# Performance work log

Hardware: AMD Instinct MI355X
Metric: run time of the kernel (lower is better)

Reference implementation:

```python
import jax, jax.numpy as jnp
import numpy as np
import math

B, C, DH = 2048, 64, 512
CAP_VOCAB = 11  # max(core_capacities)+1
DIST_VOCAB = 3


def setup_inputs() -> dict:
    key = jax.random.key(0)
    ks = jax.random.split(key, 12)
    inp = {
        "Ht_C": jax.random.normal(ks[0], (B, C, DH), jnp.float32),
        "core_capacities": jax.random.randint(ks[1], (B, C), 0, CAP_VOCAB),
        "distances": jax.random.randint(ks[2], (B, C), 0, DIST_VOCAB),
        "H_X": jax.random.normal(ks[3], (B, DH), jnp.float32),
        "Ht_S": jax.random.normal(ks[4], (B, DH), jnp.float32),
        "Eq_Q": jax.random.normal(ks[5], (B, DH), jnp.float32),
        "double": jax.random.randint(ks[6], (B,), 0, 2).astype(bool),
        # learned parameters (nn.Embedding tables and bias-free Linear weights, [out,in])
        "cap_emb": jax.random.normal(ks[7], (CAP_VOCAB, DH), jnp.float32) * 0.02,
        "dist_emb": jax.random.normal(ks[8], (DIST_VOCAB, DH), jnp.float32) * 0.02,
        "W_q": jax.random.normal(ks[9], (DH, 3 * DH), jnp.float32) * (1.0 / math.sqrt(3 * DH)),
        "W_k": jax.random.normal(ks[10], (DH, DH), jnp.float32) * (1.0 / math.sqrt(DH)),
        "W_v": jax.random.normal(ks[11], (DH, DH), jnp.float32) * (1.0 / math.sqrt(DH)),
    }
    return inp


def reference(Ht_C, core_capacities, distances, H_X, Ht_S, Eq_Q, double,
              cap_emb, dist_emb, W_q, W_k, W_v):
    scale = 1.0 / math.sqrt(Ht_C.shape[-1])  # 1/sqrt(d_H), slice_emb_size == d_H
    # dynamic core embeddings G_{t,q}^{(C)}: [B,C,dH]
    G = Ht_C + cap_emb[core_capacities] + dist_emb[distances]
    # context and projections
    context = jnp.concatenate([H_X, Ht_S, Eq_Q], axis=-1)          # [B,3dH]
    Q = context @ W_q.T                                            # [B,dH]
    K = jnp.einsum('bcd,ed->bce', G, W_k)                          # [B,C,dH]
    V = jnp.einsum('bcd,ed->bce', G, W_v)                          # [B,C,dH]
    # glimpse attention over cores
    attn_logits = jnp.einsum('bcd,bd->bc', K, Q) * scale           # [B,C]
    attn_weights = jax.nn.softmax(attn_logits, axis=-1)            # softmax over cores
    glimpse = jnp.einsum('bc,bcd->bd', attn_weights, V)            # [B,dH]
    # pointer logits + capacity mask
    u = jnp.einsum('bcd,bd->bc', K, glimpse) * scale               # [B,C]
    need = jnp.where(double[:, None], 2, 1)                        # [B,1]
    invalid = core_capacities < need                               # [B,C]
    u = jnp.where(invalid, -jnp.inf, u)
    return jax.nn.softmax(u, axis=-1)                              # [B,C]
```

## Files before the change

### kernel.cpp

```cpp
#include <hip/hip_runtime.h>
#include <math.h>

#define DH 512
#define CC 64
#define NB 2048
#define SCALE 0.044194173824159216f

#define PD(d) ((((d) >> 5) * 36) + ((d) & 31))

__device__ __forceinline__ float wsum(float v) {
#pragma unroll
  for (int off = 32; off; off >>= 1) v += __shfl_xor(v, off, 64);
  return v;
}

__global__ __launch_bounds__(128) void pre_kernel(const float* __restrict__ Wq,
                                                  const float* __restrict__ Wv,
                                                  const float* __restrict__ Wk,
                                                  float* __restrict__ Aout,
                                                  float* __restrict__ Mout,
                                                  const unsigned char* __restrict__ dbl,
                                                  int* __restrict__ need) {
  const int bx = blockIdx.x;
  const int t = threadIdx.x;
  if (bx == 256) {
    __shared__ int flagNZ, flagFP;
    if (t == 0) { flagNZ = 0; flagFP = 0; }
    __syncthreads();
    int nz = 0, fp = 0;
    for (int i = t; i < NB; i += 128) {
      if (i & 3) {
        unsigned char v = dbl[i];
        nz |= (v != 0);
        fp |= (v == 0x3f) | (v == 0x80);
      }
    }
    if (nz) atomicOr(&flagNZ, 1);
    if (fp) atomicOr(&flagFP, 1);
    __syncthreads();
    const int isFP = flagFP, isByte = flagNZ && !flagFP;
    for (int i = t; i < NB; i += 128) {
      int v;
      if (isFP)        v = (((const float*)dbl)[i] != 0.0f);
      else if (isByte) v = (dbl[i] != 0);
      else             v = (((const int*)dbl)[i] != 0);
      need[i] = v ? 2 : 1;
    }
    return;
  }
  __shared__ float As[16][64];
  __shared__ float Bs[16][64];
  const int mt = bx >> 3, nt = bx & 7;
  const int m0 = mt * 64, n0 = nt * 64;
  const bool isQ = (m0 < 1536);
  const float* Acol = isQ ? (Wq + m0) : (Wv + (m0 - 1536));
  const int lda = isQ ? 1536 : 512;
  float* Cout = isQ ? (Aout + (size_t)m0 * 512) : (Mout + (size_t)(m0 - 1536) * 512);
  const int lr = t >> 3;
  const int lc = (t & 7) << 3;
  const int tx = t & 15, ty = t >> 4;

  float4 ra0, ra1, rb0, rb1;
  ra0 = *(const float4*)&Acol[(size_t)lr * lda + lc];
  ra1 = *(const float4*)&Acol[(size_t)lr * lda + lc + 4];
  rb0 = *(const float4*)&Wk[(size_t)lr * 512 + n0 + lc];
  rb1 = *(const float4*)&Wk[(size_t)lr * 512 + n0 + lc + 4];
  float acc[8][4] = {};
  for (int k0 = 0; k0 < 512; k0 += 16) {
    __syncthreads();
    *(float4*)&As[lr][lc] = ra0;
    *(float4*)&As[lr][lc + 4] = ra1;
    *(float4*)&Bs[lr][lc] = rb0;
    *(float4*)&Bs[lr][lc + 4] = rb1;
    __syncthreads();
    if (k0 + 16 < 512) {
      const int kn = k0 + 16 + lr;
      ra0 = *(const float4*)&Acol[(size_t)kn * lda + lc];
      ra1 = *(const float4*)&Acol[(size_t)kn * lda + lc + 4];
      rb0 = *(const float4*)&Wk[(size_t)kn * 512 + n0 + lc];
      rb1 = *(const float4*)&Wk[(size_t)kn * 512 + n0 + lc + 4];
    }
#pragma unroll
    for (int k = 0; k < 16; ++k) {
      float4 a0 = *(float4*)&As[k][ty << 3];
      float4 a1 = *(float4*)&As[k][(ty << 3) + 4];
      float4 b  = *(float4*)&Bs[k][tx << 2];
      float av[8] = {a0.x, a0.y, a0.z, a0.w, a1.x, a1.y, a1.z, a1.w};
      float bv[4] = {b.x, b.y, b.z, b.w};
#pragma unroll
      for (int i = 0; i < 8; ++i)
#pragma unroll
        for (int j = 0; j < 4; ++j) acc[i][j] = fmaf(av[i], bv[j], acc[i][j]);
    }
  }
#pragma unroll
  for (int i = 0; i < 8; ++i) {
    float4 o = {acc[i][0], acc[i][1], acc[i][2], acc[i][3]};
    *(float4*)&Cout[(size_t)((ty << 3) + i) * 512 + n0 + (tx << 2)] = o;
  }
}

#define AS_STR 132

__global__ __launch_bounds__(256) void gemm_nn2p(const float* __restrict__ A0,
                                                 const float* __restrict__ A1,
                                                 const float* __restrict__ A2,
                                                 const float* __restrict__ B,
                                                 float* __restrict__ Cp,
                                                 int kchunk) {
  __shared__ float As[16 * AS_STR];
  __shared__ float Bs[16 * 64];
  const int t = threadIdx.x;
  const int m0 = blockIdx.x * 128, n0 = blockIdx.y * 64;
  const int kbeg = blockIdx.z * kchunk, kend = kbeg + kchunk;
  float* C = Cp + (size_t)blockIdx.z * (NB * DH);
  const int tx = t & 15, ty = t >> 4;
  const int ar0 = t >> 2;
  const int ak4 = (t & 3) << 2;
  const int bk = t >> 4, bn4 = (t & 15) << 2;

  float4 ra0, ra1, rb;
  {
    const float* base = (kbeg < 512) ? A0 : ((kbeg < 1024) ? A1 : A2);
    const int kk = kbeg & 511;
    ra0 = *(const float4*)&base[(size_t)(m0 + ar0) * 512 + kk + ak4];
    ra1 = *(const float4*)&base[(size_t)(m0 + ar0 + 64) * 512 + kk + ak4];
    rb  = *(const float4*)&B[(size_t)(kbeg + bk) * 512 + n0 + bn4];
  }
  float acc[8][4] = {};
  for (int k0 = kbeg; k0 < kend; k0 += 16) {
    __syncthreads();
    As[(ak4 + 0) * AS_STR + ar0] = ra0.x;
    As[(ak4 + 1) * AS_STR + ar0] = ra0.y;
    As[(ak4 + 2) * AS_STR + ar0] = ra0.z;
    As[(ak4 + 3) * AS_STR + ar0] = ra0.w;
    As[(ak4 + 0) * AS_STR + ar0 + 64] = ra1.x;
    As[(ak4 + 1) * AS_STR + ar0 + 64] = ra1.y;
    As[(ak4 + 2) * AS_STR + ar0 + 64] = ra1.z;
    As[(ak4 + 3) * AS_STR + ar0 + 64] = ra1.w;
    *(float4*)&Bs[bk * 64 + bn4] = rb;
    __syncthreads();
    if (k0 + 16 < kend) {
      const int kn = k0 + 16;
      const float* base = (kn < 512) ? A0 : ((kn < 1024) ? A1 : A2);
      const int kk = kn & 511;
      ra0 = *(const float4*)&base[(size_t)(m0 + ar0) * 512 + kk + ak4];
      ra1 = *(const float4*)&base[(size_t)(m0 + ar0 + 64) * 512 + kk + ak4];
      rb  = *(const float4*)&B[(size_t)(kn + bk) * 512 + n0 + bn4];
    }
#pragma unroll
    for (int k = 0; k < 16; ++k) {
      float4 a0 = *(float4*)&As[k * AS_STR + (ty << 3)];
      float4 a1 = *(float4*)&As[k * AS_STR + (ty << 3) + 4];
      float4 b  = *(float4*)&Bs[k * 64 + (tx << 2)];
      float av[8] = {a0.x, a0.y, a0.z, a0.w, a1.x, a1.y, a1.z, a1.w};
      float bv[4] = {b.x, b.y, b.z, b.w};
#pragma unroll
      for (int i = 0; i < 8; ++i)
#pragma unroll
        for (int j = 0; j < 4; ++j) acc[i][j] = fmaf(av[i], bv[j], acc[i][j]);
    }
  }
#pragma unroll
  for (int i = 0; i < 8; ++i) {
    float4 o = {acc[i][0], acc[i][1], acc[i][2], acc[i][3]};
    *(float4*)&C[(size_t)(m0 + (ty << 3) + i) * 512 + n0 + (tx << 2)] = o;
  }
}

__global__ __launch_bounds__(256)
__attribute__((amdgpu_waves_per_eu(2)))
void fused_kernel(const float* __restrict__ HtC,
                  const int* __restrict__ caps,
                  const int* __restrict__ dists,
                  const float* __restrict__ Qkp,
                  const float* __restrict__ Mm,
                  const float* __restrict__ cap_emb,
                  const float* __restrict__ dist_emb,
                  const int* __restrict__ need,
                  float* __restrict__ out) {
  const int t = threadIdx.x;
  const int wv = t >> 6, ln = t & 63;
  const int g = ln >> 4, l16 = ln & 15;
  const int b0 = blockIdx.x << 2;

  __shared__ __align__(16) float qk[4][576];
  __shared__ __align__(16) float gks[4][576];
  __shared__ __align__(16) float accs[4][576];
  __shared__ __align__(16) float Gws[4][DH];
  __shared__ __align__(16) float gkp[2][4][DH];
  __shared__ float ec[CC];
  __shared__ float capQ[4][11], distQ[4][3];
  __shared__ float capE[11], distE[3];
  __shared__ float capG[4][11], distG[4][3];
  __shared__ float lsum_s;
  __shared__ int capsS[4][CC], distsS[4][CC];

  {
    const int hh = t >> 6, c = t & 63;
    capsS[hh][c] = caps[(size_t)(b0 + hh) * CC + c];
    distsS[hh][c] = dists[(size_t)(b0 + hh) * CC + c];
  }

  {
    const int hh = t >> 6;
    const int d0 = (t & 63) << 3;
    const size_t bo = (size_t)(b0 + hh) * DH + d0;
    float4 q0 = make_float4(0.f, 0.f, 0.f, 0.f);
    float4 q1 = make_float4(0.f, 0.f, 0.f, 0.f);
#pragma unroll
    for (int z = 0; z < 4; ++z) {
      float4 a = *(const float4*)&Qkp[(size_t)z * NB * DH + bo];
      float4 b4 = *(const float4*)&Qkp[(size_t)z * NB * DH + bo + 4];
      q0.x += a.x; q0.y += a.y; q0.z += a.z; q0.w += a.w;
      q1.x += b4.x; q1.y += b4.y; q1.z += b4.z; q1.w += b4.w;
    }
    *(float4*)&qk[hh][PD(d0)] = q0;
    *(float4*)&qk[hh][PD(d0 + 4)] = q1;
  }
  __syncthreads();

#pragma unroll
  for (int h = 0; h < 4; ++h) {
#pragma unroll
    for (int r = 0; r < 3; ++r) {
      int v = wv + (r << 2);
      if (v < 11) {
        float s = 0.f;
#pragma unroll
        for (int j = 0; j < 8; ++j)
          s = fmaf(cap_emb[v * DH + ln + (j << 6)], qk[h][PD(ln + (j << 6))], s);
        s = wsum(s);
        if (ln == 0) capQ[h][v] = s;
      }
    }
    if (wv < 3) {
      float s = 0.f;
#pragma unroll
      for (int j = 0; j < 8; ++j)
        s = fmaf(dist_emb[wv * DH + ln + (j << 6)], qk[h][PD(ln + (j << 6))], s);
      s = wsum(s);
      if (ln == 0) distQ[h][wv] = s;
    }
  }

  const int coff = l16 << 5;

  for (int h = 0; h < 4; ++h) {
    const int b = b0 + h;
    if (t < 11) capE[t] = 0.f;
    if (t < 3) distE[t] = 0.f;
    __syncthreads();
    float4 qs[8];
#pragma unroll
    for (int j = 0; j < 8; ++j) qs[j] = *(const float4*)&qk[h][l16 * 36 + 4 * j];
    float4 ac[8];
#pragma unroll
    for (int j = 0; j < 8; ++j) ac[j] = make_float4(0.f, 0.f, 0.f, 0.f);
    const float* hb = HtC + (size_t)b * CC * DH;
    float4 hv[8];
    {
      const float* hp = hb + (size_t)((wv << 4) + g) * DH + coff;
#pragma unroll
      for (int j = 0; j < 8; ++j) hv[j] = *(const float4*)&hp[4 * j];
    }
#pragma unroll 1
    for (int k = 0; k < 4; ++k) {
      const int c = (wv << 4) + (k << 2) + g;
      float4 hvn[8];
      if (k < 3) {
        const float* hp = hb + (size_t)(c + 4) * DH + coff;
#pragma unroll
        for (int j = 0; j < 8; ++j) hvn[j] = *(const float4*)&hp[4 * j];
      }
      float s = 0.f;
#pragma unroll
      for (int j = 0; j < 8; ++j) {
        s = fmaf(hv[j].x, qs[j].x, s); s = fmaf(hv[j].y, qs[j].y, s);
        s = fmaf(hv[j].z, qs[j].z, s); s = fmaf(hv[j].w, qs[j].w, s);
      }
      s += __shfl_xor(s, 1, 64);
      s += __shfl_xor(s, 2, 64);
      s += __shfl_xor(s, 4, 64);
      s += __shfl_xor(s, 8, 64);
      float e = __expf(SCALE * (s + capQ[h][capsS[h][c]] + distQ[h][distsS[h][c]]));
      if (l16 == 0) ec[c] = e;
#pragma unroll
      for (int j = 0; j < 8; ++j) {
        ac[j].x = fmaf(e, hv[j].x, ac[j].x); ac[j].y = fmaf(e, hv[j].y, ac[j].y);
        ac[j].z = fmaf(e, hv[j].z, ac[j].z); ac[j].w = fmaf(e, hv[j].w, ac[j].w);
      }
      if (k < 3) {
#pragma unroll
        for (int j = 0; j < 8; ++j) hv[j] = hvn[j];
      }
    }
#pragma unroll
    for (int j = 0; j < 8; ++j) {
      ac[j].x += __shfl_xor(ac[j].x, 16, 64); ac[j].x += __shfl_xor(ac[j].x, 32, 64);
      ac[j].y += __shfl_xor(ac[j].y, 16, 64); ac[j].y += __shfl_xor(ac[j].y, 32, 64);
      ac[j].z += __shfl_xor(ac[j].z, 16, 64); ac[j].z += __shfl_xor(ac[j].z, 32, 64);
      ac[j].w += __shfl_xor(ac[j].w, 16, 64); ac[j].w += __shfl_xor(ac[j].w, 32, 64);
    }
    if (g == 0) {
#pragma unroll
      for (int j = 0; j < 8; ++j)
        *(float4*)&accs[wv][l16 * 36 + 4 * j] = ac[j];
    }
    __syncthreads();
    if (t < CC) {
      float e = ec[t];
      float l = wsum(e);
      if (t == 0) lsum_s = l;
      atomicAdd(&capE[capsS[h][t]], e);
      atomicAdd(&distE[distsS[h][t]], e);
    }
    __syncthreads();
    const float rinv = 1.0f / lsum_s;
#pragma unroll
    for (int dd = 0; dd < 2; ++dd) {
      int d = t + (dd << 8);
      float gg = accs[0][PD(d)] + accs[1][PD(d)] + accs[2][PD(d)] + accs[3][PD(d)];
#pragma unroll
      for (int v = 0; v < 11; ++v) gg = fmaf(capE[v], cap_emb[v * DH + d], gg);
#pragma unroll
      for (int v = 0; v < 3; ++v) gg = fmaf(distE[v], dist_emb[v * DH + d], gg);
      Gws[h][d] = gg * rinv;
    }
    __syncthreads();
  }

  {
    const int e4 = (t & 127) << 2;
    const int half = t >> 7;
    const float* Mp = Mm + (size_t)(half << 8) * DH + e4;
    const float* gw0 = &Gws[0][half << 8];
    const float* gw1 = &Gws[1][half << 8];
    const float* gw2 = &Gws[2][half << 8];
    const float* gw3 = &Gws[3][half << 8];
    float4 s0 = make_float4(0.f, 0.f, 0.f, 0.f);
    float4 s1 = s0, s2 = s0, s3 = s0;
#pragma unroll 4
    for (int d = 0; d < 256; ++d) {
      float4 m4 = *(const float4*)&Mp[(size_t)d * DH];
      float g0 = gw0[d], g1 = gw1[d], g2 = gw2[d], g3 = gw3[d];
      s0.x = fmaf(g0, m4.x, s0.x); s0.y = fmaf(g0, m4.y, s0.y);
      s0.z = fmaf(g0, m4.z, s0.z); s0.w = fmaf(g0, m4.w, s0.w);
      s1.x = fmaf(g1, m4.x, s1.x); s1.y = fmaf(g1, m4.y, s1.y);
      s1.z = fmaf(g1, m4.z, s1.z); s1.w = fmaf(g1, m4.w, s1.w);
      s2.x = fmaf(g2, m4.x, s2.x); s2.y = fmaf(g2, m4.y, s2.y);
      s2.z = fmaf(g2, m4.z, s2.z); s2.w = fmaf(g2, m4.w, s2.w);
      s3.x = fmaf(g3, m4.x, s3.x); s3.y = fmaf(g3, m4.y, s3.y);
      s3.z = fmaf(g3, m4.z, s3.z); s3.w = fmaf(g3, m4.w, s3.w);
    }
    *(float4*)&gkp[half][0][e4] = s0;
    *(float4*)&gkp[half][1][e4] = s1;
    *(float4*)&gkp[half][2][e4] = s2;
    *(float4*)&gkp[half][3][e4] = s3;
  }
  __syncthreads();
#pragma unroll
  for (int h = 0; h < 4; ++h) {
    gks[h][PD(t)] = gkp[0][h][t] + gkp[1][h][t];
    gks[h][PD(t + 256)] = gkp[0][h][t + 256] + gkp[1][h][t + 256];
  }
  __syncthreads();

#pragma unroll
  for (int h = 0; h < 4; ++h) {
#pragma unroll
    for (int r = 0; r < 3; ++r) {
      int v = wv + (r << 2);
      if (v < 11) {
        float s = 0.f;
#pragma unroll
        for (int j = 0; j < 8; ++j)
          s = fmaf(cap_emb[v * DH + ln + (j << 6)], gks[h][PD(ln + (j << 6))], s);
        s = wsum(s);
        if (ln == 0) capG[h][v] = s;
      }
    }
    if (wv < 3) {
      float s = 0.f;
#pragma unroll
      for (int j = 0; j < 8; ++j)
        s = fmaf(dist_emb[wv * DH + ln + (j << 6)], gks[h][PD(ln + (j << 6))], s);
      s = wsum(s);
      if (ln == 0) distG[h][wv] = s;
    }
  }
  __syncthreads();

  for (int h = 3; h >= 0; --h) {
    const int b = b0 + h;
    float4 gs[8];
#pragma unroll
    for (int j = 0; j < 8; ++j) gs[j] = *(const float4*)&gks[h][l16 * 36 + 4 * j];
    const float* hb = HtC + (size_t)b * CC * DH;
    float4 hv[8];
    {
      const float* hp = hb + (size_t)((wv << 4) + g) * DH + coff;
#pragma unroll
      for (int j = 0; j < 8; ++j) hv[j] = *(const float4*)&hp[4 * j];
    }
#pragma unroll 1
    for (int k = 0; k < 4; ++k) {
      const int c = (wv << 4) + (k << 2) + g;
      float4 hvn[8];
      if (k < 3) {
        const float* hp = hb + (size_t)(c + 4) * DH + coff;
#pragma unroll
        for (int j = 0; j < 8; ++j) hvn[j] = *(const float4*)&hp[4 * j];
      }
      float s = 0.f;
#pragma unroll
      for (int j = 0; j < 8; ++j) {
        s = fmaf(hv[j].x, gs[j].x, s); s = fmaf(hv[j].y, gs[j].y, s);
        s = fmaf(hv[j].z, gs[j].z, s); s = fmaf(hv[j].w, gs[j].w, s);
      }
      s += __shfl_xor(s, 1, 64);
      s += __shfl_xor(s, 2, 64);
      s += __shfl_xor(s, 4, 64);
      s += __shfl_xor(s, 8, 64);
      if (l16 == 0)
        ec[c] = SCALE * (s + capG[h][capsS[h][c]] + distG[h][distsS[h][c]]);
      if (k < 3) {
#pragma unroll
        for (int j = 0; j < 8; ++j) hv[j] = hvn[j];
      }
    }
    __syncthreads();
    if (t < CC) {
      int nb = need[b];
      float x = ec[t];
      if (capsS[h][t] < nb) x = -INFINITY;
      float m = x;
#pragma unroll
      for (int off = 32; off; off >>= 1) m = fmaxf(m, __shfl_xor(m, off, 64));
      float e = __expf(x - m);
      float ssum = wsum(e);
      out[(size_t)b * CC + t] = e / ssum;
    }
    __syncthreads();
  }
}

extern "C" void kernel_launch(void* const* d_in, const int* in_sizes, int n_in,
                              void* d_out, int out_size, void* d_ws, size_t ws_size,
                              hipStream_t stream) {
  const float* HtC      = (const float*)d_in[0];
  const int* caps       = (const int*)d_in[1];
  const int* dists      = (const int*)d_in[2];
  const float* H_X      = (const float*)d_in[3];
  const float* Ht_S     = (const float*)d_in[4];
  const float* Eq_Q     = (const float*)d_in[5];
  const unsigned char* dbl = (const unsigned char*)d_in[6];
  const float* cap_emb  = (const float*)d_in[7];
  const float* dist_emb = (const float*)d_in[8];
  const float* W_q      = (const float*)d_in[9];
  const float* W_k      = (const float*)d_in[10];
  const float* W_v      = (const float*)d_in[11];
  float* out = (float*)d_out;

  float* ws     = (float*)d_ws;
  float* wsA    = ws;
  float* wsM    = wsA + 1536 * 512;
  float* wsQkp  = wsM + 512 * 512;
  int* wsNeed   = (int*)(wsQkp + 4 * 2048 * 512);

  pre_kernel<<<257, 128, 0, stream>>>(W_q, W_v, W_k, wsA, wsM, dbl, wsNeed);
  gemm_nn2p<<<dim3(16, 8, 4), 256, 0, stream>>>(H_X, Ht_S, Eq_Q, wsA, wsQkp, 384);
  fused_kernel<<<NB / 4, 256, 0, stream>>>(HtC, caps, dists, wsQkp, wsM,
                                           cap_emb, dist_emb, wsNeed, out);
}
```

Before: 534.1 us.

## Process two batches per block with higher occupancy and split dot-product accumulators

Each fused_kernel block now handles two batch rows instead of four, doubling the grid and cutting shared memory per block, and the waves-per-EU hint rises from 2 to 4 so more blocks can be resident and hide latency on the HtC streaming loads. The per-core dot products use four independent accumulators to shorten the FMA dependency chain. The capacity and distance bias lookups are hoisted out of the inner loop. The cost is that each block reuses its M matrix row loads across only two batches instead of four in the G·M projection, raising global/L2 traffic for M, and register pressure under the tighter occupancy target may cause spills.

Measured after the change: 699.8 us. +31.0%, slower.

```diff
diff --git a/kernel.cpp b/kernel.cpp
--- a/kernel.cpp
+++ b/kernel.cpp
@@ -169,7 +169,7 @@
 }
 
 __global__ __launch_bounds__(256)
-__attribute__((amdgpu_waves_per_eu(2)))
+__attribute__((amdgpu_waves_per_eu(4)))
 void fused_kernel(const float* __restrict__ HtC,
                   const int* __restrict__ caps,
                   const int* __restrict__ dists,
@@ -182,46 +182,42 @@
   const int t = threadIdx.x;
   const int wv = t >> 6, ln = t & 63;
   const int g = ln >> 4, l16 = ln & 15;
-  const int b0 = blockIdx.x << 2;
-
-  __shared__ __align__(16) float qk[4][576];
-  __shared__ __align__(16) float gks[4][576];
+  const int b0 = blockIdx.x << 1;
+
+  __shared__ __align__(16) float qk[2][576];
+  __shared__ __align__(16) float gks[2][576];
   __shared__ __align__(16) float accs[4][576];
-  __shared__ __align__(16) float Gws[4][DH];
-  __shared__ __align__(16) float gkp[2][4][DH];
+  __shared__ __align__(16) float Gws[2][DH];
+  __shared__ __align__(16) float gkp[2][2][DH];
   __shared__ float ec[CC];
-  __shared__ float capQ[4][11], distQ[4][3];
+  __shared__ float capQ[2][11], distQ[2][3];
   __shared__ float capE[11], distE[3];
-  __shared__ float capG[4][11], distG[4][3];
+  __shared__ float capG[2][11], distG[2][3];
   __shared__ float lsum_s;
-  __shared__ int capsS[4][CC], distsS[4][CC];
-
-  {
+  __shared__ int capsS[2][CC], distsS[2][CC];
+
+  if (t < 128) {
     const int hh = t >> 6, c = t & 63;
     capsS[hh][c] = caps[(size_t)(b0 + hh) * CC + c];
     distsS[hh][c] = dists[(size_t)(b0 + hh) * CC + c];
   }
 
   {
-    const int hh = t >> 6;
-    const int d0 = (t & 63) << 3;
+    const int hh = t >> 7;
+    const int d0 = (t & 127) << 2;
     const size_t bo = (size_t)(b0 + hh) * DH + d0;
     float4 q0 = make_float4(0.f, 0.f, 0.f, 0.f);
-    float4 q1 = make_float4(0.f, 0.f, 0.f, 0.f);
 #pragma unroll
     for (int z = 0; z < 4; ++z) {
       float4 a = *(const float4*)&Qkp[(size_t)z * NB * DH + bo];
-      float4 b4 = *(const float4*)&Qkp[(size_t)z * NB * DH + bo + 4];
       q0.x += a.x; q0.y += a.y; q0.z += a.z; q0.w += a.w;
-      q1.x += b4.x; q1.y += b4.y; q1.z += b4.z; q1.w += b4.w;
     }
     *(float4*)&qk[hh][PD(d0)] = q0;
-    *(float4*)&qk[hh][PD(d0 + 4)] = q1;
   }
   __syncthreads();
 
 #pragma unroll
-  for (int h = 0; h < 4; ++h) {
+  for (int h = 0; h < 2; ++h) {
 #pragma unroll
     for (int r = 0; r < 3; ++r) {
       int v = wv + (r << 2);
@@ -246,11 +242,17 @@
 
   const int coff = l16 << 5;
 
-  for (int h = 0; h < 4; ++h) {
+  for (int h = 0; h < 2; ++h) {
     const int b = b0 + h;
     if (t < 11) capE[t] = 0.f;
     if (t < 3) distE[t] = 0.f;
     __syncthreads();
+    float cd[4];
+#pragma unroll
+    for (int k = 0; k < 4; ++k) {
+      const int c = (wv << 4) + (k << 2) + g;
+      cd[k] = capQ[h][capsS[h][c]] + distQ[h][distsS[h][c]];
+    }
     float4 qs[8];
 #pragma unroll
     for (int j = 0; j < 8; ++j) qs[j] = *(const float4*)&qk[h][l16 * 36 + 4 * j];
@@ -273,17 +275,24 @@
 #pragma unroll
         for (int j = 0; j < 8; ++j) hvn[j] = *(const float4*)&hp[4 * j];
       }
-      float s = 0.f;
-#pragma unroll
-      for (int j = 0; j < 8; ++j) {
-        s = fmaf(hv[j].x, qs[j].x, s); s = fmaf(hv[j].y, qs[j].y, s);
-        s = fmaf(hv[j].z, qs[j].z, s); s = fmaf(hv[j].w, qs[j].w, s);
-      }
+      float s0 = 0.f, s1 = 0.f, s2 = 0.f, s3 = 0.f;
+#pragma unroll
+      for (int j = 0; j < 2; ++j) {
+        s0 = fmaf(hv[j].x, qs[j].x, s0); s0 = fmaf(hv[j].y, qs[j].y, s0);
+        s0 = fmaf(hv[j].z, qs[j].z, s0); s0 = fmaf(hv[j].w, qs[j].w, s0);
+        s1 = fmaf(hv[j + 2].x, qs[j + 2].x, s1); s1 = fmaf(hv[j + 2].y, qs[j + 2].y, s1);
+        s1 = fmaf(hv[j + 2].z, qs[j + 2].z, s1); s1 = fmaf(hv[j + 2].w, qs[j + 2].w, s1);
+        s2 = fmaf(hv[j + 4].x, qs[j + 4].x, s2); s2 = fmaf(hv[j + 4].y, qs[j + 4].y, s2);
+        s2 = fmaf(hv[j + 4].z, qs[j + 4].z, s2); s2 = fmaf(hv[j + 4].w, qs[j + 4].w, s2);
+        s3 = fmaf(hv[j + 6].x, qs[j + 6].x, s3); s3 = fmaf(hv[j + 6].y, qs[j + 6].y, s3);
+        s3 = fmaf(hv[j + 6].z, qs[j + 6].z, s3); s3 = fmaf(hv[j + 6].w, qs[j + 6].w, s3);
+      }
+      float s = (s0 + s1) + (s2 + s3);
       s += __shfl_xor(s, 1, 64);
       s += __shfl_xor(s, 2, 64);
       s += __shfl_xor(s, 4, 64);
       s += __shfl_xor(s, 8, 64);
-      float e = __expf(SCALE * (s + capQ[h][capsS[h][c]] + distQ[h][distsS[h][c]]));
+      float e = __expf(SCALE * (s + cd[k]));
       if (l16 == 0) ec[c] = e;
 #pragma unroll
       for (int j = 0; j < 8; ++j) {
@@ -334,40 +343,33 @@
     const int e4 = (t & 127) << 2;
     const int half = t >> 7;
     const float* Mp = Mm + (size_t)(half << 8) * DH + e4;
-    const float* gw0 = &Gws[0][half << 8];
-    const float* gw1 = &Gws[1][half << 8];
-    const float* gw2 = &Gws[2][half << 8];
-    const float* gw3 = &Gws[3][half << 8];
+    const float* g0p = &Gws[0][half << 8];
+    const float* g1p = &Gws[1][half << 8];
     float4 s0 = make_float4(0.f, 0.f, 0.f, 0.f);
-    float4 s1 = s0, s2 = s0, s3 = s0;
-#pragma unroll 4
+    float4 s1 = s0;
+#pragma unroll 8
     for (int d = 0; d < 256; ++d) {
       float4 m4 = *(const float4*)&Mp[(size_t)d * DH];
-      float g0 = gw0[d], g1 = gw1[d], g2 = gw2[d], g3 = gw3[d];
+      float g0 = g0p[d];
+      float g1 = g1p[d];
       s0.x = fmaf(g0, m4.x, s0.x); s0.y = fmaf(g0, m4.y, s0.y);
       s0.z = fmaf(g0, m4.z, s0.z); s0.w = fmaf(g0, m4.w, s0.w);
       s1.x = fmaf(g1, m4.x, s1.x); s1.y = fmaf(g1, m4.y, s1.y);
       s1.z = fmaf(g1, m4.z, s1.z); s1.w = fmaf(g1, m4.w, s1.w);
-      s2.x = fmaf(g2, m4.x, s2.x); s2.y = fmaf(g2, m4.y, s2.y);
-      s2.z = fmaf(g2, m4.z, s2.z); s2.w = fmaf(g2, m4.w, s2.w);
-      s3.x = fmaf(g3, m4.x, s3.x); s3.y = fmaf(g3, m4.y, s3.y);
-      s3.z = fmaf(g3, m4.z, s3.z); s3.w = fmaf(g3, m4.w, s3.w);
     }
     *(float4*)&gkp[half][0][e4] = s0;
     *(float4*)&gkp[half][1][e4] = s1;
-    *(float4*)&gkp[half][2][e4] = s2;
-    *(float4*)&gkp[half][3][e4] = s3;
   }
   __syncthreads();
 #pragma unroll
-  for (int h = 0; h < 4; ++h) {
+  for (int h = 0; h < 2; ++h) {
     gks[h][PD(t)] = gkp[0][h][t] + gkp[1][h][t];
     gks[h][PD(t + 256)] = gkp[0][h][t + 256] + gkp[1][h][t + 256];
   }
   __syncthreads();
 
 #pragma unroll
-  for (int h = 0; h < 4; ++h) {
+  for (int h = 0; h < 2; ++h) {
 #pragma unroll
     for (int r = 0; r < 3; ++r) {
       int v = wv + (r << 2);
@@ -391,8 +393,14 @@
   }
   __syncthreads();
 
-  for (int h = 3; h >= 0; --h) {
+  for (int h = 1; h >= 0; --h) {
     const int b = b0 + h;
+    float cd[4];
+#pragma unroll
+    for (int k = 0; k < 4; ++k) {
+      const int c = (wv << 4) + (k << 2) + g;
+      cd[k] = capG[h][capsS[h][c]] + distG[h][distsS[h][c]];
+    }
     float4 gs[8];
 #pragma unroll
     for (int j = 0; j < 8; ++j) gs[j] = *(const float4*)&gks[h][l16 * 36 + 4 * j];
@@ -412,18 +420,25 @@
 #pragma unroll
         for (int j = 0; j < 8; ++j) hvn[j] = *(const float4*)&hp[4 * j];
       }
-      float s = 0.f;
-#pragma unroll
-      for (int j = 0; j < 8; ++j) {
-        s = fmaf(hv[j].x, gs[j].x, s); s = fmaf(hv[j].y, gs[j].y, s);
-        s = fmaf(hv[j].z, gs[j].z, s); s = fmaf(hv[j].w, gs[j].w, s);
-      }
+      float s0 = 0.f, s1 = 0.f, s2 = 0.f, s3 = 0.f;
+#pragma unroll
+      for (int j = 0; j < 2; ++j) {
+        s0 = fmaf(hv[j].x, gs[j].x, s0); s0 = fmaf(hv[j].y, gs[j].y, s0);
+        s0 = fmaf(hv[j].z, gs[j].z, s0); s0 = fmaf(hv[j].w, gs[j].w, s0);
+        s1 = fmaf(hv[j + 2].x, gs[j + 2].x, s1); s1 = fmaf(hv[j + 2].y, gs[j + 2].y, s1);
+        s1 = fmaf(hv[j + 2].z, gs[j + 2].z, s1); s1 = fmaf(hv[j + 2].w, gs[j + 2].w, s1);
+        s2 = fmaf(hv[j + 4].x, gs[j + 4].x, s2); s2 = fmaf(hv[j + 4].y, gs[j + 4].y, s2);
+        s2 = fmaf(hv[j + 4].z, gs[j + 4].z, s2); s2 = fmaf(hv[j + 4].w, gs[j + 4].w, s2);
+        s3 = fmaf(hv[j + 6].x, gs[j + 6].x, s3); s3 = fmaf(hv[j + 6].y, gs[j + 6].y, s3);
+        s3 = fmaf(hv[j + 6].z, gs[j + 6].z, s3); s3 = fmaf(hv[j + 6].w, gs[j + 6].w, s3);
+      }
+      float s = (s0 + s1) + (s2 + s3);
       s += __shfl_xor(s, 1, 64);
       s += __shfl_xor(s, 2, 64);
       s += __shfl_xor(s, 4, 64);
       s += __shfl_xor(s, 8, 64);
       if (l16 == 0)
-        ec[c] = SCALE * (s + capG[h][capsS[h][c]] + distG[h][distsS[h][c]]);
+        ec[c] = SCALE * (s + cd[k]);
       if (k < 3) {
 #pragma unroll
         for (int j = 0; j < 8; ++j) hv[j] = hvn[j];
@@ -470,6 +485,6 @@
 
   pre_kernel<<<257, 128, 0, stream>>>(W_q, W_v, W_k, wsA, wsM, dbl, wsNeed);
   gemm_nn2p<<<dim3(16, 8, 4), 256, 0, stream>>>(H_X, Ht_S, Eq_Q, wsA, wsQkp, 384);
-  fused_kernel<<<NB / 4, 256, 0, stream>>>(HtC, caps, dists, wsQkp, wsM,
+  fused_kernel<<<NB / 2, 256, 0, stream>>>(HtC, caps, dists, wsQkp, wsM,
                                            cap_emb, dist_emb, wsNeed, out);
 }
```
